# Optimization experiments

Measured on AMD Instinct MI355X. Metric: run time of the kernel, lower is better.

Reference implementation:

```python
import jax, jax.numpy as jnp
import numpy as np

EPS = 1e-06

def setup_inputs() -> dict:
    key = jax.random.key(0)
    k1, k2, k3, k4, k5 = jax.random.split(key, 5)
    B, T, D, Dv = 4, 2048, 128, 128
    q = jax.random.normal(k1, (B, T, D), dtype=jnp.float32)
    k = jax.random.normal(k2, (B, T, D), dtype=jnp.float32)
    v = jax.random.normal(k3, (B, T, Dv), dtype=jnp.float32)
    # phi = nn.Linear(dim, dim) followed by ELU; torch Linear default init ~ U(-1/sqrt(D), 1/sqrt(D))
    lim = 1.0 / np.sqrt(D)
    W_phi = jax.random.uniform(k4, (D, D), minval=-lim, maxval=lim, dtype=jnp.float32)
    b_phi = jax.random.uniform(k5, (D,), minval=-lim, maxval=lim, dtype=jnp.float32)
    return {"q": q, "k": k, "v": v, "W_phi": W_phi, "b_phi": b_phi}

def reference(q, k, v, W_phi, b_phi):
    # feature map: phi(x) = ELU(x @ W^T + b) + 1  (positive features)
    def phi(x):
        return jax.nn.elu(jnp.einsum('btd,ed->bte', x, W_phi) + b_phi) + 1.0

    Q = phi(q)                      # [B,T,D]
    K = phi(k)                      # [B,T,D]
    # causal recurrent state (zero initial state since h=None):
    # z_t = sum_{tau<=t} K_tau                 -> [B,T,D]
    # s_t = sum_{tau<=t} K_tau (outer) v_tau   -> [B,T,D,Dv]
    z = jnp.cumsum(K, axis=1)
    s = jnp.cumsum(K[..., :, None] * v[..., None, :], axis=1)
    den = jnp.einsum('btd,btd->bt', Q, z) + EPS          # [B,T]
    out = jnp.einsum('btd,btde->bte', Q, s) / den[..., None]  # [B,T,Dv]
    return out
```

## Files before the change

kernel.cpp:

```cpp
#include <hip/hip_runtime.h>
#include <hip/hip_bf16.h>

#define BB 4
#define TT 2048
#define DD 128
#define CHK 64
#define NCHK 32
#define NCHKS (BB*NCHK)

typedef __attribute__((ext_vector_type(8))) short  bf16x8;
typedef __attribute__((ext_vector_type(4))) float  f32x4;

#define MFMA(a,b,c) __builtin_amdgcn_mfma_f32_16x16x32_bf16(a, b, c, 0, 0, 0)

__device__ __forceinline__ short f2b(float f) {
    union { float f; unsigned u; } x; x.f = f;
    unsigned r = x.u + 0x7fffu + ((x.u >> 16) & 1u);
    return (short)(r >> 16);
}
__device__ __forceinline__ float b2f(short s) {
    union { unsigned u; float f; } x; x.u = ((unsigned)(unsigned short)s) << 16;
    return x.f;
}
__device__ __forceinline__ bf16x8 cvt8(const float* p) {
    float4 a = *(const float4*)p, b = *(const float4*)(p + 4);
    bf16x8 r;
    r[0]=f2b(a.x); r[1]=f2b(a.y); r[2]=f2b(a.z); r[3]=f2b(a.w);
    r[4]=f2b(b.x); r[5]=f2b(b.y); r[6]=f2b(b.z); r[7]=f2b(b.w);
    return r;
}

__device__ __forceinline__ void w_to_lds(const float* __restrict__ W,
                                         short (*Wl)[DD + 8], int tid) {
    #pragma unroll
    for (int it = 0; it < 16; ++it) {
        int i = tid + it * 256;
        int row = i >> 5, c4 = (i & 31) * 4;
        float4 v = *(const float4*)(W + (size_t)row * DD + c4);
        unsigned lo = (unsigned short)f2b(v.x) | ((unsigned)(unsigned short)f2b(v.y) << 16);
        unsigned hi = (unsigned short)f2b(v.z) | ((unsigned)(unsigned short)f2b(v.w) << 16);
        uint2 p; p.x = lo; p.y = hi;
        *(uint2*)&Wl[row][c4] = p;
    }
}

__global__ __launch_bounds__(256) void k1_chunk(const float* __restrict__ kin,
                                                const float* __restrict__ vin,
                                                const float* __restrict__ W,
                                                const float* __restrict__ bias,
                                                float* __restrict__ SsT_g,
                                                float* __restrict__ zc_g,
                                                short* __restrict__ vT_g) {
    int c = blockIdx.x >> 1, h = blockIdx.x & 1;
    const float* kc = kin + (size_t)c * CHK * DD;
    const float* vc = vin + (size_t)c * CHK * DD;

    __shared__ __align__(16) short Wl [DD][DD + 8];
    __shared__ __align__(16) short KfT[DD][CHK + 8];
    __shared__ __align__(16) short vT [CHK][CHK + 8];
    __shared__ __align__(16) float SsT[CHK][DD + 4];

    int tid = threadIdx.x, lane = tid & 63, w = tid >> 6;
    int l15 = lane & 15, l4 = lane >> 4;
    const f32x4 z4 = {0.f, 0.f, 0.f, 0.f};

    bf16x8 af[4];
    {
        int row = 16 * w + l15;
        #pragma unroll
        for (int kk = 0; kk < 4; ++kk)
            af[kk] = cvt8(kc + row * DD + kk * 32 + l4 * 8);
    }
    w_to_lds(W, Wl, tid);
    #pragma unroll
    for (int it = 0; it < 4; ++it) {
        int i = tid + it * 256;
        int t = i >> 4, c4 = (i & 15) * 4;
        float4 vv = *(const float4*)(vc + t * DD + 64 * h + c4);
        vT[c4 + 0][t] = f2b(vv.x); vT[c4 + 1][t] = f2b(vv.y);
        vT[c4 + 2][t] = f2b(vv.z); vT[c4 + 3][t] = f2b(vv.w);
    }
    __syncthreads();

    #pragma unroll
    for (int n = 0; n < 8; ++n) {
        int e = 16 * n + l15;
        f32x4 d = z4;
        #pragma unroll
        for (int kk = 0; kk < 4; ++kk) {
            bf16x8 bw = *(const bf16x8*)&Wl[e][kk * 32 + l4 * 8];
            d = MFMA(af[kk], bw, d);
        }
        float bv = bias[e];
        #pragma unroll
        for (int j = 0; j < 4; ++j) {
            float zv = d[j] + bv;
            float r = (zv > 0.f) ? (zv + 1.f) : __expf(zv);
            KfT[e][16 * w + l4 * 4 + j] = f2b(r);
        }
    }
    __syncthreads();

    if (h == 0 && tid < DD) {
        float s = 0.f;
        #pragma unroll
        for (int t8 = 0; t8 < CHK / 8; ++t8) {
            bf16x8 kv = *(const bf16x8*)&KfT[tid][t8 * 8];
            #pragma unroll
            for (int j = 0; j < 8; ++j) s += b2f(kv[j]);
        }
        zc_g[(size_t)c * DD + tid] = s;
    }

    #pragma unroll
    for (int it = 0; it < 2; ++it) {
        int i = tid + it * 256;
        int e = i >> 3, t0 = (i & 7) * 8;
        *(bf16x8*)(vT_g + (size_t)c * DD * CHK + (64 * h + e) * CHK + t0) =
            *(const bf16x8*)&vT[e][t0];
    }

    {
        f32x4 sacc[2][4];
        #pragma unroll
        for (int mi = 0; mi < 2; ++mi)
            #pragma unroll
            for (int n = 0; n < 4; ++n) sacc[mi][n] = z4;
        #pragma unroll
        for (int kk = 0; kk < 2; ++kk) {
            bf16x8 afr[2];
            #pragma unroll
            for (int mi = 0; mi < 2; ++mi)
                afr[mi] = *(const bf16x8*)&KfT[16 * (2 * w + mi) + l15][kk * 32 + l4 * 8];
            #pragma unroll
            for (int n = 0; n < 4; ++n) {
                bf16x8 bfr = *(const bf16x8*)&vT[16 * n + l15][kk * 32 + l4 * 8];
                sacc[0][n] = MFMA(afr[0], bfr, sacc[0][n]);
                sacc[1][n] = MFMA(afr[1], bfr, sacc[1][n]);
            }
        }
        #pragma unroll
        for (int mi = 0; mi < 2; ++mi)
            #pragma unroll
            for (int n = 0; n < 4; ++n) {
                int e = 16 * n + l15;
                #pragma unroll
                for (int j = 0; j < 4; ++j)
                    SsT[e][16 * (2 * w + mi) + l4 * 4 + j] = sacc[mi][n][j];
            }
    }
    __syncthreads();

    float* dst = SsT_g + (size_t)c * DD * DD + (size_t)64 * h * DD;
    #pragma unroll
    for (int it = 0; it < 8; ++it) {
        int i = tid + it * 256;
        int e = i >> 5, c4 = (i & 31) * 4;
        *(float4*)(dst + e * DD + c4) = *(const float4*)&SsT[e][c4];
    }
}

__global__ __launch_bounds__(128) void k2_scan(const float* __restrict__ SsT_g,
                                               const float* __restrict__ zc_g,
                                               short* __restrict__ SpT_g,
                                               float* __restrict__ zp_g) {
    int e = blockIdx.x & 127, b = blockIdx.x >> 7;
    int d = threadIdx.x;
    size_t base = ((size_t)(b * NCHK) * DD + e) * DD + d;
    const size_t stride = (size_t)DD * DD;

    float vals[NCHK];
    #pragma unroll
    for (int c2 = 0; c2 < NCHK; ++c2) vals[c2] = SsT_g[base + c2 * stride];
    float run = 0.f;
    #pragma unroll
    for (int c2 = 0; c2 < NCHK; ++c2) {
        SpT_g[base + c2 * stride] = f2b(run);
        run += vals[c2];
    }
    if (e == 0) {
        float vz[NCHK];
        #pragma unroll
        for (int c2 = 0; c2 < NCHK; ++c2) vz[c2] = zc_g[(size_t)(b * NCHK + c2) * DD + d];
        float rz = 0.f;
        #pragma unroll
        for (int c2 = 0; c2 < NCHK; ++c2) {
            zp_g[(size_t)(b * NCHK + c2) * DD + d] = rz;
            rz += vz[c2];
        }
    }
}

__global__ __launch_bounds__(256) void k3_out(const float* __restrict__ q,
                                              const float* __restrict__ kin,
                                              const float* __restrict__ W,
                                              const float* __restrict__ bias,
                                              const short* __restrict__ SpT_g,
                                              const float* __restrict__ zp_g,
                                              const short* __restrict__ vT_g,
                                              float* __restrict__ out) {
    int c = blockIdx.x >> 1, h = blockIdx.x & 1;

    __shared__ __align__(16) short Wl[DD][DD + 8];
    __shared__ __align__(16) short Qf[CHK][DD + 8];
    __shared__ __align__(16) short Kf[CHK][DD + 8];
    __shared__ __align__(16) short Ps[CHK][CHK + 8];
    __shared__ float zs[DD];
    __shared__ float den[CHK];

    int tid = threadIdx.x, lane = tid & 63, w = tid >> 6;
    int l15 = lane & 15, l4 = lane >> 4;
    const f32x4 z4 = {0.f, 0.f, 0.f, 0.f};

    if (tid < DD) zs[tid] = zp_g[(size_t)c * DD + tid];

    const float* qc = q   + (size_t)c * CHK * DD;
    const float* kc = kin + (size_t)c * CHK * DD;
    bf16x8 afq[4], afk[4];
    {
        int row = 16 * w + l15;
        #pragma unroll
        for (int kk = 0; kk < 4; ++kk) {
            afq[kk] = cvt8(qc + row * DD + kk * 32 + l4 * 8);
            afk[kk] = cvt8(kc + row * DD + kk * 32 + l4 * 8);
        }
    }
    w_to_lds(W, Wl, tid);
    __syncthreads();

    #pragma unroll
    for (int n = 0; n < 8; ++n) {
        int e = 16 * n + l15;
        f32x4 dq = z4, dk = z4;
        #pragma unroll
        for (int kk = 0; kk < 4; ++kk) {
            bf16x8 bw = *(const bf16x8*)&Wl[e][kk * 32 + l4 * 8];
            dq = MFMA(afq[kk], bw, dq);
            dk = MFMA(afk[kk], bw, dk);
        }
        float bv = bias[e];
        #pragma unroll
        for (int j = 0; j < 4; ++j) {
            int t = 16 * w + l4 * 4 + j;
            float zq = dq[j] + bv;
            Qf[t][e] = f2b((zq > 0.f) ? (zq + 1.f) : __expf(zq));
            float zk = dk[j] + bv;
            Kf[t][e] = f2b((zk > 0.f) ? (zk + 1.f) : __expf(zk));
        }
    }
    __syncthreads();

    bf16x8 aq[4];
    #pragma unroll
    for (int kk = 0; kk < 4; ++kk)
        aq[kk] = *(const bf16x8*)&Qf[16 * w + l15][kk * 32 + l4 * 8];
    #pragma unroll
    for (int n2 = 0; n2 < 4; ++n2) {
        f32x4 p = z4;
        #pragma unroll
        for (int kk = 0; kk < 4; ++kk) {
            bf16x8 bk = *(const bf16x8*)&Kf[16 * n2 + l15][kk * 32 + l4 * 8];
            p = MFMA(aq[kk], bk, p);
        }
        int t2 = 16 * n2 + l15;
        #pragma unroll
        for (int j = 0; j < 4; ++j) {
            int t = 16 * w + l4 * 4 + j;
            Ps[t][t2] = (t2 <= t) ? f2b(p[j]) : (short)0;
        }
    }
    __syncthreads();

    if (tid < CHK) {
        float s = 1e-6f;
        #pragma unroll
        for (int t8 = 0; t8 < CHK / 8; ++t8) {
            bf16x8 pv = *(const bf16x8*)&Ps[tid][t8 * 8];
            #pragma unroll
            for (int j = 0; j < 8; ++j) s += b2f(pv[j]);
        }
        #pragma unroll
        for (int d8 = 0; d8 < DD / 8; ++d8) {
            bf16x8 qv = *(const bf16x8*)&Qf[tid][d8 * 8];
            #pragma unroll
            for (int j = 0; j < 8; ++j) s += b2f(qv[j]) * zs[d8 * 8 + j];
        }
        den[tid] = s;
    }

    bf16x8 ap[2];
    #pragma unroll
    for (int kk = 0; kk < 2; ++kk)
        ap[kk] = *(const bf16x8*)&Ps[16 * w + l15][kk * 32 + l4 * 8];

    const short* Sp  = SpT_g + (size_t)c * DD * DD;
    const short* vTg = vT_g + (size_t)c * DD * CHK;
    f32x4 oacc[4];
    #pragma unroll
    for (int n = 0; n < 4; ++n) oacc[n] = z4;
    #pragma unroll
    for (int n = 0; n < 4; ++n) {
        int e = 64 * h + 16 * n + l15;
        #pragma unroll
        for (int kk = 0; kk < 4; ++kk) {
            bf16x8 bs = *(const bf16x8*)(Sp + e * DD + kk * 32 + l4 * 8);
            oacc[n] = MFMA(aq[kk], bs, oacc[n]);
        }
        #pragma unroll
        for (int kk = 0; kk < 2; ++kk) {
            bf16x8 bv = *(const bf16x8*)(vTg + e * CHK + kk * 32 + l4 * 8);
            oacc[n] = MFMA(ap[kk], bv, oacc[n]);
        }
    }
    __syncthreads();

    float* oc = out + (size_t)c * CHK * DD;
    float invs[4];
    #pragma unroll
    for (int j = 0; j < 4; ++j) invs[j] = 1.0f / den[16 * w + l4 * 4 + j];
    #pragma unroll
    for (int n = 0; n < 4; ++n) {
        int e = 64 * h + 16 * n + l15;
        #pragma unroll
        for (int j = 0; j < 4; ++j) {
            int t = 16 * w + l4 * 4 + j;
            oc[t * DD + e] = oacc[n][j] * invs[j];
        }
    }
}

extern "C" void kernel_launch(void* const* d_in, const int* in_sizes, int n_in,
                              void* d_out, int out_size, void* d_ws, size_t ws_size,
                              hipStream_t stream) {
    const float* q  = (const float*)d_in[0];
    const float* k  = (const float*)d_in[1];
    const float* v  = (const float*)d_in[2];
    const float* W  = (const float*)d_in[3];
    const float* bi = (const float*)d_in[4];
    float* out = (float*)d_out;

    float* SsT_g = (float*)d_ws;
    float* zc_g  = SsT_g + (size_t)NCHKS * DD * DD;
    float* zp_g  = zc_g + (size_t)NCHKS * DD;
    short* SpT_g = (short*)(zp_g + (size_t)NCHKS * DD);
    short* vT_g  = SpT_g + (size_t)NCHKS * DD * DD;

    k1_chunk<<<2 * NCHKS, 256, 0, stream>>>(k, v, W, bi, SsT_g, zc_g, vT_g);
    k2_scan<<<512, 128, 0, stream>>>(SsT_g, zc_g, SpT_g, zp_g);
    k3_out<<<2 * NCHKS, 256, 0, stream>>>(q, k, W, bi, SpT_g, zp_g, vT_g, out);
}
```

Baseline: 29.17 us.

## Move feature-map computation into chunk kernel and split output kernel finer

The chunk kernel now computes phi(q) and phi(k) once, using its two half-blocks, and writes them to global memory as bf16. The output kernel therefore no longer reloads W or recomputes the features, and it runs with four blocks per chunk instead of two. Chunk states are stored in bf16 instead of fp32, which halves that traffic through the scan. The denominator is now computed with an MFMA against zp and a shuffle reduction, replacing a serial per-row loop. The costs are extra global writes of Qf and Kf, each block recomputing the causal P matrix four times, and lower precision in the intermediate states.

```diff
diff --git a/kernel.cpp b/kernel.cpp
--- a/kernel.cpp
+++ b/kernel.cpp
@@ -30,8 +30,40 @@
     return r;
 }
 
-__device__ __forceinline__ void w_to_lds(const float* __restrict__ W,
-                                         short (*Wl)[DD + 8], int tid) {
+__global__ __launch_bounds__(256) void k1_chunk(const float* __restrict__ q,
+                                                const float* __restrict__ kin,
+                                                const float* __restrict__ vin,
+                                                const float* __restrict__ W,
+                                                const float* __restrict__ bias,
+                                                short* __restrict__ Ss_g,
+                                                float* __restrict__ zc_g,
+                                                short* __restrict__ vT_g,
+                                                short* __restrict__ Qf_g,
+                                                short* __restrict__ Kf_g) {
+    int c = blockIdx.x >> 1, h = blockIdx.x & 1;
+    const float* qc = q   + (size_t)c * CHK * DD;
+    const float* kc = kin + (size_t)c * CHK * DD;
+    const float* vc = vin + (size_t)c * CHK * DD;
+
+    __shared__ __align__(16) short Wl  [DD][DD + 8];
+    __shared__ __align__(16) short KfT [DD][CHK + 8];
+    __shared__ __align__(16) short vT  [CHK][CHK + 8];
+    __shared__ __align__(16) short stage[CHK][DD + 8];
+
+    int tid = threadIdx.x, lane = tid & 63, w = tid >> 6;
+    int l15 = lane & 15, l4 = lane >> 4;
+    const f32x4 z4 = {0.f, 0.f, 0.f, 0.f};
+
+    bf16x8 afk[4], afq[4];
+    {
+        int row = 16 * w + l15;
+        #pragma unroll
+        for (int kk = 0; kk < 4; ++kk) afk[kk] = cvt8(kc + row * DD + kk * 32 + l4 * 8);
+        if (h) {
+            #pragma unroll
+            for (int kk = 0; kk < 4; ++kk) afq[kk] = cvt8(qc + row * DD + kk * 32 + l4 * 8);
+        }
+    }
     #pragma unroll
     for (int it = 0; it < 16; ++it) {
         int i = tid + it * 256;
@@ -42,36 +74,6 @@
         uint2 p; p.x = lo; p.y = hi;
         *(uint2*)&Wl[row][c4] = p;
     }
-}
-
-__global__ __launch_bounds__(256) void k1_chunk(const float* __restrict__ kin,
-                                                const float* __restrict__ vin,
-                                                const float* __restrict__ W,
-                                                const float* __restrict__ bias,
-                                                float* __restrict__ SsT_g,
-                                                float* __restrict__ zc_g,
-                                                short* __restrict__ vT_g) {
-    int c = blockIdx.x >> 1, h = blockIdx.x & 1;
-    const float* kc = kin + (size_t)c * CHK * DD;
-    const float* vc = vin + (size_t)c * CHK * DD;
-
-    __shared__ __align__(16) short Wl [DD][DD + 8];
-    __shared__ __align__(16) short KfT[DD][CHK + 8];
-    __shared__ __align__(16) short vT [CHK][CHK + 8];
-    __shared__ __align__(16) float SsT[CHK][DD + 4];
-
-    int tid = threadIdx.x, lane = tid & 63, w = tid >> 6;
-    int l15 = lane & 15, l4 = lane >> 4;
-    const f32x4 z4 = {0.f, 0.f, 0.f, 0.f};
-
-    bf16x8 af[4];
-    {
-        int row = 16 * w + l15;
-        #pragma unroll
-        for (int kk = 0; kk < 4; ++kk)
-            af[kk] = cvt8(kc + row * DD + kk * 32 + l4 * 8);
-    }
-    w_to_lds(W, Wl, tid);
     #pragma unroll
     for (int it = 0; it < 4; ++it) {
         int i = tid + it * 256;
@@ -89,18 +91,47 @@
         #pragma unroll
         for (int kk = 0; kk < 4; ++kk) {
             bf16x8 bw = *(const bf16x8*)&Wl[e][kk * 32 + l4 * 8];
-            d = MFMA(af[kk], bw, d);
+            d = MFMA(afk[kk], bw, d);
         }
         float bv = bias[e];
         #pragma unroll
         for (int j = 0; j < 4; ++j) {
             float zv = d[j] + bv;
-            float r = (zv > 0.f) ? (zv + 1.f) : __expf(zv);
-            KfT[e][16 * w + l4 * 4 + j] = f2b(r);
-        }
-    }
-    __syncthreads();
-
+            short r = f2b((zv > 0.f) ? (zv + 1.f) : __expf(zv));
+            int t = 16 * w + l4 * 4 + j;
+            KfT[e][t] = r;
+            if (h == 0) stage[t][e] = r;
+        }
+    }
+    if (h) {
+        #pragma unroll
+        for (int n = 0; n < 8; ++n) {
+            int e = 16 * n + l15;
+            f32x4 d = z4;
+            #pragma unroll
+            for (int kk = 0; kk < 4; ++kk) {
+                bf16x8 bw = *(const bf16x8*)&Wl[e][kk * 32 + l4 * 8];
+                d = MFMA(afq[kk], bw, d);
+            }
+            float bv = bias[e];
+            #pragma unroll
+            for (int j = 0; j < 4; ++j) {
+                float zv = d[j] + bv;
+                stage[16 * w + l4 * 4 + j][e] = f2b((zv > 0.f) ? (zv + 1.f) : __expf(zv));
+            }
+        }
+    }
+    __syncthreads();
+
+    {
+        short* dst = (h ? Qf_g : Kf_g) + (size_t)c * CHK * DD;
+        #pragma unroll
+        for (int it = 0; it < 4; ++it) {
+            int i = tid + it * 256;
+            int t = i >> 4, u = (i & 15) * 8;
+            *(bf16x8*)(dst + t * DD + u) = *(const bf16x8*)&stage[t][u];
+        }
+    }
     if (h == 0 && tid < DD) {
         float s = 0.f;
         #pragma unroll
@@ -111,7 +142,6 @@
         }
         zc_g[(size_t)c * DD + tid] = s;
     }
-
     #pragma unroll
     for (int it = 0; it < 2; ++it) {
         int i = tid + it * 256;
@@ -120,49 +150,51 @@
             *(const bf16x8*)&vT[e][t0];
     }
 
+    f32x4 sacc[2][4];
+    #pragma unroll
+    for (int mi = 0; mi < 2; ++mi)
+        #pragma unroll
+        for (int n = 0; n < 4; ++n) sacc[mi][n] = z4;
+    #pragma unroll
+    for (int kk = 0; kk < 2; ++kk) {
+        bf16x8 afr[2];
+        #pragma unroll
+        for (int mi = 0; mi < 2; ++mi)
+            afr[mi] = *(const bf16x8*)&KfT[16 * (2 * w + mi) + l15][kk * 32 + l4 * 8];
+        #pragma unroll
+        for (int n = 0; n < 4; ++n) {
+            bf16x8 bfr = *(const bf16x8*)&vT[16 * n + l15][kk * 32 + l4 * 8];
+            sacc[0][n] = MFMA(afr[0], bfr, sacc[0][n]);
+            sacc[1][n] = MFMA(afr[1], bfr, sacc[1][n]);
+        }
+    }
+    __syncthreads();
+
+    #pragma unroll
+    for (int mi = 0; mi < 2; ++mi)
+        #pragma unroll
+        for (int n = 0; n < 4; ++n) {
+            int e = 16 * n + l15;
+            #pragma unroll
+            for (int j = 0; j < 4; ++j)
+                stage[e][16 * (2 * w + mi) + l4 * 4 + j] = f2b(sacc[mi][n][j]);
+        }
+    __syncthreads();
+
     {
-        f32x4 sacc[2][4];
-        #pragma unroll
-        for (int mi = 0; mi < 2; ++mi)
-            #pragma unroll
-            for (int n = 0; n < 4; ++n) sacc[mi][n] = z4;
-        #pragma unroll
-        for (int kk = 0; kk < 2; ++kk) {
-            bf16x8 afr[2];
-            #pragma unroll
-            for (int mi = 0; mi < 2; ++mi)
-                afr[mi] = *(const bf16x8*)&KfT[16 * (2 * w + mi) + l15][kk * 32 + l4 * 8];
-            #pragma unroll
-            for (int n = 0; n < 4; ++n) {
-                bf16x8 bfr = *(const bf16x8*)&vT[16 * n + l15][kk * 32 + l4 * 8];
-                sacc[0][n] = MFMA(afr[0], bfr, sacc[0][n]);
-                sacc[1][n] = MFMA(afr[1], bfr, sacc[1][n]);
-            }
-        }
-        #pragma unroll
-        for (int mi = 0; mi < 2; ++mi)
-            #pragma unroll
-            for (int n = 0; n < 4; ++n) {
-                int e = 16 * n + l15;
-                #pragma unroll
-                for (int j = 0; j < 4; ++j)
-                    SsT[e][16 * (2 * w + mi) + l4 * 4 + j] = sacc[mi][n][j];
-            }
-    }
-    __syncthreads();
-
-    float* dst = SsT_g + (size_t)c * DD * DD + (size_t)64 * h * DD;
-    #pragma unroll
-    for (int it = 0; it < 8; ++it) {
-        int i = tid + it * 256;
-        int e = i >> 5, c4 = (i & 31) * 4;
-        *(float4*)(dst + e * DD + c4) = *(const float4*)&SsT[e][c4];
-    }
-}
-
-__global__ __launch_bounds__(128) void k2_scan(const float* __restrict__ SsT_g,
+        short* dst = Ss_g + (size_t)c * DD * DD + (size_t)(64 * h) * DD;
+        #pragma unroll
+        for (int it = 0; it < 4; ++it) {
+            int i = tid + it * 256;
+            int e = i >> 4, u = (i & 15) * 8;
+            *(bf16x8*)(dst + e * DD + u) = *(const bf16x8*)&stage[e][u];
+        }
+    }
+}
+
+__global__ __launch_bounds__(128) void k2_scan(const short* __restrict__ Ss_g,
                                                const float* __restrict__ zc_g,
-                                               short* __restrict__ SpT_g,
+                                               short* __restrict__ Sp_g,
                                                float* __restrict__ zp_g) {
     int e = blockIdx.x & 127, b = blockIdx.x >> 7;
     int d = threadIdx.x;
@@ -171,11 +203,11 @@
 
     float vals[NCHK];
     #pragma unroll
-    for (int c2 = 0; c2 < NCHK; ++c2) vals[c2] = SsT_g[base + c2 * stride];
+    for (int c2 = 0; c2 < NCHK; ++c2) vals[c2] = b2f(Ss_g[base + c2 * stride]);
     float run = 0.f;
     #pragma unroll
     for (int c2 = 0; c2 < NCHK; ++c2) {
-        SpT_g[base + c2 * stride] = f2b(run);
+        Sp_g[base + c2 * stride] = f2b(run);
         run += vals[c2];
     }
     if (e == 0) {
@@ -191,116 +223,83 @@
     }
 }
 
-__global__ __launch_bounds__(256) void k3_out(const float* __restrict__ q,
-                                              const float* __restrict__ kin,
-                                              const float* __restrict__ W,
-                                              const float* __restrict__ bias,
-                                              const short* __restrict__ SpT_g,
+__global__ __launch_bounds__(256) void k3_out(const short* __restrict__ Qf_g,
+                                              const short* __restrict__ Kf_g,
+                                              const short* __restrict__ Sp_g,
                                               const float* __restrict__ zp_g,
                                               const short* __restrict__ vT_g,
                                               float* __restrict__ out) {
-    int c = blockIdx.x >> 1, h = blockIdx.x & 1;
-
-    __shared__ __align__(16) short Wl[DD][DD + 8];
-    __shared__ __align__(16) short Qf[CHK][DD + 8];
-    __shared__ __align__(16) short Kf[CHK][DD + 8];
+    int c = blockIdx.x >> 2, h2 = blockIdx.x & 3;
+
     __shared__ __align__(16) short Ps[CHK][CHK + 8];
-    __shared__ float zs[DD];
     __shared__ float den[CHK];
 
     int tid = threadIdx.x, lane = tid & 63, w = tid >> 6;
     int l15 = lane & 15, l4 = lane >> 4;
     const f32x4 z4 = {0.f, 0.f, 0.f, 0.f};
 
-    if (tid < DD) zs[tid] = zp_g[(size_t)c * DD + tid];
-
-    const float* qc = q   + (size_t)c * CHK * DD;
-    const float* kc = kin + (size_t)c * CHK * DD;
-    bf16x8 afq[4], afk[4];
-    {
-        int row = 16 * w + l15;
+    const short* Qc = Qf_g + (size_t)c * CHK * DD;
+    const short* Kc = Kf_g + (size_t)c * CHK * DD;
+    const float* zp = zp_g + (size_t)c * DD;
+
+    bf16x8 aq[4];
+    #pragma unroll
+    for (int kk = 0; kk < 4; ++kk)
+        aq[kk] = *(const bf16x8*)(Qc + (16 * w + l15) * DD + kk * 32 + l4 * 8);
+
+    bf16x8 bz[4];
+    #pragma unroll
+    for (int kk = 0; kk < 4; ++kk) {
+        bf16x8 zf = cvt8(zp + kk * 32 + l4 * 8);
+        bf16x8 zero = {0,0,0,0,0,0,0,0};
+        bz[kk] = (l15 == 0) ? zf : zero;
+    }
+
+    float rs[4] = {0.f, 0.f, 0.f, 0.f};
+    f32x4 p4 = z4;
+    #pragma unroll
+    for (int kk = 0; kk < 4; ++kk) p4 = MFMA(aq[kk], bz[kk], p4);
+    #pragma unroll
+    for (int n2 = 0; n2 < 4; ++n2) {
+        f32x4 p = z4;
         #pragma unroll
         for (int kk = 0; kk < 4; ++kk) {
-            afq[kk] = cvt8(qc + row * DD + kk * 32 + l4 * 8);
-            afk[kk] = cvt8(kc + row * DD + kk * 32 + l4 * 8);
-        }
-    }
-    w_to_lds(W, Wl, tid);
-    __syncthreads();
-
-    #pragma unroll
-    for (int n = 0; n < 8; ++n) {
-        int e = 16 * n + l15;
-        f32x4 dq = z4, dk = z4;
-        #pragma unroll
-        for (int kk = 0; kk < 4; ++kk) {
-            bf16x8 bw = *(const bf16x8*)&Wl[e][kk * 32 + l4 * 8];
-            dq = MFMA(afq[kk], bw, dq);
-            dk = MFMA(afk[kk], bw, dk);
-        }
-        float bv = bias[e];
+            bf16x8 bk = *(const bf16x8*)(Kc + (16 * n2 + l15) * DD + kk * 32 + l4 * 8);
+            p = MFMA(aq[kk], bk, p);
+        }
+        int t2 = 16 * n2 + l15;
         #pragma unroll
         for (int j = 0; j < 4; ++j) {
             int t = 16 * w + l4 * 4 + j;
-            float zq = dq[j] + bv;
-            Qf[t][e] = f2b((zq > 0.f) ? (zq + 1.f) : __expf(zq));
-            float zk = dk[j] + bv;
-            Kf[t][e] = f2b((zk > 0.f) ? (zk + 1.f) : __expf(zk));
-        }
-    }
-    __syncthreads();
-
-    bf16x8 aq[4];
-    #pragma unroll
-    for (int kk = 0; kk < 4; ++kk)
-        aq[kk] = *(const bf16x8*)&Qf[16 * w + l15][kk * 32 + l4 * 8];
-    #pragma unroll
-    for (int n2 = 0; n2 < 4; ++n2) {
-        f32x4 p = z4;
-        #pragma unroll
-        for (int kk = 0; kk < 4; ++kk) {
-            bf16x8 bk = *(const bf16x8*)&Kf[16 * n2 + l15][kk * 32 + l4 * 8];
-            p = MFMA(aq[kk], bk, p);
-        }
-        int t2 = 16 * n2 + l15;
-        #pragma unroll
-        for (int j = 0; j < 4; ++j) {
-            int t = 16 * w + l4 * 4 + j;
-            Ps[t][t2] = (t2 <= t) ? f2b(p[j]) : (short)0;
-        }
-    }
-    __syncthreads();
-
-    if (tid < CHK) {
-        float s = 1e-6f;
-        #pragma unroll
-        for (int t8 = 0; t8 < CHK / 8; ++t8) {
-            bf16x8 pv = *(const bf16x8*)&Ps[tid][t8 * 8];
-            #pragma unroll
-            for (int j = 0; j < 8; ++j) s += b2f(pv[j]);
-        }
-        #pragma unroll
-        for (int d8 = 0; d8 < DD / 8; ++d8) {
-            bf16x8 qv = *(const bf16x8*)&Qf[tid][d8 * 8];
-            #pragma unroll
-            for (int j = 0; j < 8; ++j) s += b2f(qv[j]) * zs[d8 * 8 + j];
-        }
-        den[tid] = s;
-    }
+            float pm = (t2 <= t) ? p[j] : 0.f;
+            Ps[t][t2] = f2b(pm);
+            rs[j] += pm;
+        }
+    }
+    #pragma unroll
+    for (int off = 1; off < 16; off <<= 1) {
+        #pragma unroll
+        for (int j = 0; j < 4; ++j) rs[j] += __shfl_xor(rs[j], off);
+    }
+    if (l15 == 0) {
+        #pragma unroll
+        for (int j = 0; j < 4; ++j)
+            den[16 * w + l4 * 4 + j] = rs[j] + p4[j] + 1e-6f;
+    }
+    __syncthreads();
 
     bf16x8 ap[2];
     #pragma unroll
     for (int kk = 0; kk < 2; ++kk)
         ap[kk] = *(const bf16x8*)&Ps[16 * w + l15][kk * 32 + l4 * 8];
 
-    const short* Sp  = SpT_g + (size_t)c * DD * DD;
+    const short* Sp  = Sp_g + (size_t)c * DD * DD;
     const short* vTg = vT_g + (size_t)c * DD * CHK;
-    f32x4 oacc[4];
-    #pragma unroll
-    for (int n = 0; n < 4; ++n) oacc[n] = z4;
-    #pragma unroll
-    for (int n = 0; n < 4; ++n) {
-        int e = 64 * h + 16 * n + l15;
+    f32x4 oacc[2];
+    oacc[0] = z4; oacc[1] = z4;
+    #pragma unroll
+    for (int n = 0; n < 2; ++n) {
+        int e = 32 * h2 + 16 * n + l15;
         #pragma unroll
         for (int kk = 0; kk < 4; ++kk) {
             bf16x8 bs = *(const bf16x8*)(Sp + e * DD + kk * 32 + l4 * 8);
@@ -312,15 +311,14 @@
             oacc[n] = MFMA(ap[kk], bv, oacc[n]);
         }
     }
-    __syncthreads();
 
     float* oc = out + (size_t)c * CHK * DD;
     float invs[4];
     #pragma unroll
     for (int j = 0; j < 4; ++j) invs[j] = 1.0f / den[16 * w + l4 * 4 + j];
     #pragma unroll
-    for (int n = 0; n < 4; ++n) {
-        int e = 64 * h + 16 * n + l15;
+    for (int n = 0; n < 2; ++n) {
+        int e = 32 * h2 + 16 * n + l15;
         #pragma unroll
         for (int j = 0; j < 4; ++j) {
             int t = 16 * w + l4 * 4 + j;
@@ -339,13 +337,15 @@
     const float* bi = (const float*)d_in[4];
     float* out = (float*)d_out;
 
-    float* SsT_g = (float*)d_ws;
-    float* zc_g  = SsT_g + (size_t)NCHKS * DD * DD;
-    float* zp_g  = zc_g + (size_t)NCHKS * DD;
-    short* SpT_g = (short*)(zp_g + (size_t)NCHKS * DD);
-    short* vT_g  = SpT_g + (size_t)NCHKS * DD * DD;
-
-    k1_chunk<<<2 * NCHKS, 256, 0, stream>>>(k, v, W, bi, SsT_g, zc_g, vT_g);
-    k2_scan<<<512, 128, 0, stream>>>(SsT_g, zc_g, SpT_g, zp_g);
-    k3_out<<<2 * NCHKS, 256, 0, stream>>>(q, k, W, bi, SpT_g, zp_g, vT_g, out);
-}
+    float* zc_g = (float*)d_ws;
+    float* zp_g = zc_g + (size_t)NCHKS * DD;
+    short* Ss_g = (short*)(zp_g + (size_t)NCHKS * DD);
+    short* Sp_g = Ss_g + (size_t)NCHKS * DD * DD;
+    short* vT_g = Sp_g + (size_t)NCHKS * DD * DD;
+    short* Qf_g = vT_g + (size_t)NCHKS * DD * CHK;
+    short* Kf_g = Qf_g + (size_t)NCHKS * CHK * DD;
+
+    k1_chunk<<<2 * NCHKS, 256, 0, stream>>>(q, k, v, W, bi, Ss_g, zc_g, vT_g, Qf_g, Kf_g);
+    k2_scan<<<512, 128, 0, stream>>>(Ss_g, zc_g, Sp_g, zp_g);
+    k3_out<<<4 * NCHKS, 256, 0, stream>>>(Qf_g, Kf_g, Sp_g, zp_g, vT_g, out);
+}
```

New measurement: 32.10 us. 10.1% more time.
